# Kernel optimization log

Measured on AMD Instinct MI355X. Metric: run time of the kernel, lower is better.

The kernel has to match this reference:

```python
import jax, jax.numpy as jnp
import numpy as np

HEADS = 7
DIM_HEAD = 64
SCALE = DIM_HEAD ** -0.5


def setup_inputs() -> dict:
    key = jax.random.key(0)
    ks = jax.random.split(key, 6)
    b, n, dim = 8, 1024, 448
    inner = HEADS * DIM_HEAD  # 448
    x = jax.random.normal(ks[0], (b, n, dim), dtype=jnp.float32)
    w_qv = jax.random.normal(ks[1], (dim, 2 * inner), dtype=jnp.float32) * 0.02
    ext_k = jax.random.normal(ks[2], (HEADS, n, DIM_HEAD), dtype=jnp.float32)
    ext_bias = jax.random.normal(ks[3], (HEADS, n, n), dtype=jnp.float32)
    w_out = jax.random.normal(ks[4], (inner, dim), dtype=jnp.float32) * 0.02
    b_out = jnp.zeros((dim,), dtype=jnp.float32)
    return {"x": x, "w_qv": w_qv, "ext_k": ext_k, "ext_bias": ext_bias,
            "w_out": w_out, "b_out": b_out}


def reference(x, w_qv, ext_k, ext_bias, w_out, b_out):
    b, n, dim = x.shape
    qv = x @ w_qv                                   # [b, n, 2*inner]
    q, v = jnp.split(qv, 2, axis=-1)
    # b n (h d) -> b h n d
    q = q.reshape(b, n, HEADS, DIM_HEAD).transpose(0, 2, 1, 3)
    v = v.reshape(b, n, HEADS, DIM_HEAD).transpose(0, 2, 1, 3)
    # scores vs external learned key, additive bias applied BEFORE scale
    dots = (jnp.einsum('bhnd,hmd->bhnm', q, ext_k) + ext_bias[None]) * SCALE
    attn = jax.nn.softmax(dots, axis=-1)
    out = jnp.einsum('bhnm,bhmd->bhnd', attn, v)
    out = out.transpose(0, 2, 1, 3).reshape(b, n, HEADS * DIM_HEAD)
    return out @ w_out + b_out  # dropout is identity in eval mode
```

## Files before the change

kernel.cpp:

```cpp
#include <hip/hip_runtime.h>
#include <hip/hip_bf16.h>
#include <hip/hip_fp16.h>

#define BATCH 8
#define NSEQ 1024
#define DIMM 448
#define NHEAD 7
#define HDIM 64
#define MROWS (BATCH*NSEQ)
#define KDIM 448
#define SCALE_F 0.125f

typedef short short8 __attribute__((ext_vector_type(8)));
typedef float floatx16 __attribute__((ext_vector_type(16)));

#define MFMA32(a,b,c) __builtin_amdgcn_mfma_f32_32x32x16_bf16(a,b,c,0,0,0)

__device__ __forceinline__ unsigned short f2bf(float f){
    __hip_bfloat16 h = __float2bfloat16(f);
    return *reinterpret_cast<unsigned short*>(&h);
}
__device__ __forceinline__ float bf2f(unsigned short u){
    __hip_bfloat16 h; *reinterpret_cast<unsigned short*>(&h) = u;
    return __bfloat162float(h);
}
__device__ __forceinline__ float h2f(unsigned short u){
    __half h; *reinterpret_cast<unsigned short*>(&h) = u;
    return __half2float(h);
}
__device__ __forceinline__ unsigned short f2h(float f){
    __half h = __float2half(f);
    return *reinterpret_cast<unsigned short*>(&h);
}

__global__ __launch_bounds__(256)
void prep_all(const float* __restrict__ x, const float* __restrict__ ek,
              const float* __restrict__ wqv, const float* __restrict__ wout,
              const float* __restrict__ eb,
              unsigned short* __restrict__ xh, unsigned short* __restrict__ ekh,
              unsigned short* __restrict__ wqvTh, unsigned short* __restrict__ woTh,
              unsigned short* __restrict__ woTl, unsigned short* __restrict__ bp)
{
    __shared__ float T[2][64][33];
    const int bx = blockIdx.x, tid = threadIdx.x;

    if (bx < 3584) {
        int i = bx*256 + tid;
        float4 v = ((const float4*)x)[i];
        ((ushort4*)xh)[i] = make_ushort4(f2bf(v.x), f2bf(v.y), f2bf(v.z), f2bf(v.w));
    } else if (bx < 4032) {
        int i = (bx-3584)*256 + tid;
        float4 v = ((const float4*)ek)[i];
        ((ushort4*)ekh)[i] = make_ushort4(f2bf(v.x), f2bf(v.y), f2bf(v.z), f2bf(v.w));
    } else if (bx < 4228) {
        int lid = (bx-4032)*4 + (tid>>6);
        int kc = lid % 56, ng = lid / 56;
        int n = ng*64 + (tid&63);
        unsigned short h[8];
#pragma unroll
        for (int j = 0; j < 8; ++j) h[j] = f2bf(wqv[(size_t)(kc*8+j)*896 + n]);
        size_t o = (size_t)n*KDIM + kc*8;
        *(ushort4*)(wqvTh + o)     = make_ushort4(h[0],h[1],h[2],h[3]);
        *(ushort4*)(wqvTh + o + 4) = make_ushort4(h[4],h[5],h[6],h[7]);
    } else if (bx < 4340) {
        int lid = (bx-4228)*4 + (tid>>6);
        int kc = lid % 56, ng = lid / 56;
        int n = ng*64 + (tid&63);
        ushort4 h0={0,0,0,0}, h1={0,0,0,0}, l0={0,0,0,0}, l1={0,0,0,0};
        if (n < DIMM) {
            unsigned short h[8], l[8];
#pragma unroll
            for (int j = 0; j < 8; ++j) {
                float f = wout[(size_t)(kc*8+j)*DIMM + n];
                h[j] = f2bf(f); l[j] = f2bf(f - bf2f(h[j]));
            }
            h0 = make_ushort4(h[0],h[1],h[2],h[3]); h1 = make_ushort4(h[4],h[5],h[6],h[7]);
            l0 = make_ushort4(l[0],l[1],l[2],l[3]); l1 = make_ushort4(l[4],l[5],l[6],l[7]);
        }
        size_t o = (size_t)n*KDIM + kc*8;
        *(ushort4*)(woTh + o) = h0; *(ushort4*)(woTh + o + 4) = h1;
        *(ushort4*)(woTl + o) = l0; *(ushort4*)(woTl + o + 4) = l1;
    } else {
        const int sub = tid >> 7, st = tid & 127;
        const int lid = (bx-4340)*2 + sub;
        const int mt = lid & 31, qt = (lid>>5) & 15, h = lid >> 9;
#pragma unroll
        for (int it = 0; it < 4; ++it) {
            int idx = it*128 + st;
            int row = idx >> 3, c4 = (idx & 7)*4;
            float4 v = *(const float4*)(eb + ((size_t)(h*NSEQ + qt*64 + row))*NSEQ + mt*32 + c4);
            T[sub][row][c4+0]=v.x; T[sub][row][c4+1]=v.y;
            T[sub][row][c4+2]=v.z; T[sub][row][c4+3]=v.w;
        }
        __syncthreads();
        const int g2 = st >> 6, lane = st & 63;
        const int lq = lane & 31, quad = lane >> 5;
        const int q = g2*32 + lq;
        unsigned short* dst = bp + ((((size_t)h*16 + qt)*32 + mt)*4 + g2*2)*512 + lane*8;
#pragma unroll
        for (int jj = 0; jj < 2; ++jj) {
            unsigned short o[8];
#pragma unroll
            for (int t = 0; t < 8; ++t) {
                int m = (t&3) + 8*(t>>2) + 16*jj + 4*quad;
                o[t] = f2h(T[sub][q][m] * SCALE_F);
            }
            *(ushort4*)(dst + jj*512)     = make_ushort4(o[0],o[1],o[2],o[3]);
            *(ushort4*)(dst + jj*512 + 4) = make_ushort4(o[4],o[5],o[6],o[7]);
        }
    }
}

__global__ __launch_bounds__(64, 2)
void gemm1_reg(const unsigned short* __restrict__ Ah, const unsigned short* __restrict__ Bh,
               unsigned short* __restrict__ qd, unsigned short* __restrict__ vTd)
{
    const int lane = threadIdx.x;
    const int lq = lane & 31, lh = lane >> 5;
    const int m0 = blockIdx.x * 64;
    const int y  = blockIdx.y;
    const int n0 = y * 64;
    const unsigned short* aB = Ah + (size_t)(m0 + lq)*KDIM + lh*8;
    const unsigned short* bB = Bh + (size_t)(n0 + lq)*KDIM + lh*8;

    floatx16 acc[2][2] = {};
    short8 aR[2][2][2], bR[2][2][2];
#define LD1(kt, par) {                                                        \
    _Pragma("unroll") for (int fm = 0; fm < 2; ++fm)                          \
    _Pragma("unroll") for (int c = 0; c < 2; ++c) {                           \
        aR[par][fm][c] = *(const short8*)(aB + (size_t)fm*32*KDIM + (kt)*32 + c*16); \
        bR[par][fm][c] = *(const short8*)(bB + (size_t)fm*32*KDIM + (kt)*32 + c*16); } }

    LD1(0, 0)
#pragma unroll
    for (int kt = 0; kt < 14; ++kt) {
        const int par = kt & 1;
        if (kt < 13) LD1(kt+1, par^1)
#pragma unroll
        for (int c = 0; c < 2; ++c)
#pragma unroll
            for (int fm = 0; fm < 2; ++fm)
#pragma unroll
                for (int fn = 0; fn < 2; ++fn)
                    acc[fm][fn] = MFMA32(aR[par][fm][c], bR[par][fn][c], acc[fm][fn]);
    }
#undef LD1

    if (y < NHEAD) {
#pragma unroll
        for (int fm = 0; fm < 2; ++fm)
#pragma unroll
            for (int fn = 0; fn < 2; ++fn) {
                const int d = fn*32 + lq;
#pragma unroll
                for (int r = 0; r < 16; ++r) {
                    const int gm = m0 + fm*32 + (r&3) + 8*(r>>2) + 4*lh;
                    const int b = gm >> 10, ns = gm & 1023;
                    qd[((size_t)((b*NHEAD + y)*NSEQ + ns))*HDIM + d] = f2bf(acc[fm][fn][r]);
                }
            }
    } else {
        const int head = y - NHEAD;
#pragma unroll
        for (int fm = 0; fm < 2; ++fm)
#pragma unroll
            for (int fn = 0; fn < 2; ++fn) {
                const int d = fn*32 + lq;
#pragma unroll
                for (int r = 0; r < 16; ++r) {
                    const int gm = m0 + fm*32 + (r&3) + 8*(r>>2) + 4*lh;
                    const int b = gm >> 10, ns = gm & 1023;
                    vTd[((size_t)((b*NHEAD + head)*HDIM + d))*NSEQ + ns] = f2bf(acc[fm][fn][r]);
                }
            }
    }
}

__global__ __launch_bounds__(64, 2)
void attn4(const unsigned short* __restrict__ qh_g, const unsigned short* __restrict__ vTh,
           const unsigned short* __restrict__ ekh, const unsigned short* __restrict__ bp,
           unsigned short* __restrict__ aoh, unsigned short* __restrict__ aol)
{
    __shared__ unsigned short pS[1024];
    __shared__ float linv[2][32];

    const int lane = threadIdx.x;
    const int lq = lane & 31, lh = lane >> 5;
    const int qt = blockIdx.x, head = blockIdx.y, b = blockIdx.z;
    const int bh = b*NHEAD + head;

    short8 qf[2][4];
#pragma unroll
    for (int g2 = 0; g2 < 2; ++g2)
#pragma unroll
        for (int c = 0; c < 4; ++c)
            qf[g2][c] = *(const short8*)(qh_g +
                ((size_t)(bh*NSEQ) + qt*64 + g2*32 + lq)*HDIM + c*16 + lh*8);

    const unsigned short* kB = ekh + ((size_t)head*NSEQ + lq)*HDIM + lh*8;
    const unsigned short* vB = vTh + ((size_t)(bh*HDIM) + lq)*NSEQ;
    const unsigned short* bB = bp + ((size_t)(head*16 + qt))*65536 + lane*8;

    short8 kR[2][4], vR[2][4], bR[2][4];
#define PREF(J, par) { const int mm = ((J) < 32) ? (J) : 0;                    \
    _Pragma("unroll") for (int c = 0; c < 4; ++c)                              \
        kR[par][c] = *(const short8*)(kB + (size_t)mm*2048 + c*16);            \
    _Pragma("unroll") for (int c2 = 0; c2 < 2; ++c2)                           \
    _Pragma("unroll") for (int h2 = 0; h2 < 2; ++h2)                           \
        vR[par][c2*2+h2] = *(const short8*)(vB + (size_t)(h2*32)*NSEQ + mm*32 + (c2*2+lh)*8); \
    _Pragma("unroll") for (int u = 0; u < 4; ++u)                              \
        bR[par][u] = *(const short8*)(bB + ((size_t)mm*4 + u)*512); }

    floatx16 O[2][2] = {};
    float ls[2] = {0.f, 0.f};

#define SEC(J, par, nxt) {                                                     \
    PREF((J)+1, nxt)                                                           \
    _Pragma("unroll") for (int g2 = 0; g2 < 2; ++g2) {                         \
        floatx16 S = {};                                                       \
        _Pragma("unroll") for (int c = 0; c < 4; ++c)                          \
            S = MFMA32(kR[par][c], qf[g2][c], S);                              \
        _Pragma("unroll") for (int g = 0; g < 4; ++g) {                        \
            unsigned short hb[4];                                              \
            _Pragma("unroll") for (int j2 = 0; j2 < 4; ++j2) {                 \
                const int i = g*4 + j2;                                        \
                float bs = h2f((unsigned short)bR[par][g2*2 + (i>>3)][i&7]);   \
                float pv = __expf(fmaf(S[i], SCALE_F, bs));                    \
                ls[g2] += pv;  hb[j2] = f2bf(pv);                              \
            }                                                                  \
            *(ushort4*)(pS + g*256 + lq*8 + lh*4) = make_ushort4(hb[0],hb[1],hb[2],hb[3]); \
        }                                                                      \
        _Pragma("unroll") for (int c2 = 0; c2 < 2; ++c2) {                     \
            short8 pf = *(const short8*)(pS + ((c2*2+lh)*32 + lq)*8);          \
            O[g2][0] = MFMA32(pf, vR[par][c2*2+0], O[g2][0]);                  \
            O[g2][1] = MFMA32(pf, vR[par][c2*2+1], O[g2][1]);                  \
        } } }

    PREF(0, 0)
    for (int jj = 0; jj < 16; ++jj) {
        SEC(2*jj,   0, 1)
        SEC(2*jj+1, 1, 0)
    }
#undef SEC
#undef PREF

    float lt0 = ls[0] + __shfl_xor(ls[0], 32);
    float lt1 = ls[1] + __shfl_xor(ls[1], 32);
    if (lh == 0) { linv[0][lq] = 1.f/lt0; linv[1][lq] = 1.f/lt1; }

#pragma unroll
    for (int g2 = 0; g2 < 2; ++g2)
#pragma unroll
        for (int r = 0; r < 16; ++r) {
            const int qr = (r&3) + 8*(r>>2) + 4*lh;
            const float inv = linv[g2][qr];
            const size_t o = ((size_t)(b*NSEQ) + qt*64 + g2*32 + qr)*DIMM + head*HDIM + lq;
            float v0 = O[g2][0][r]*inv, v1 = O[g2][1][r]*inv;
            unsigned short h0 = f2bf(v0), h1 = f2bf(v1);
            aoh[o]      = h0;  aol[o]      = f2bf(v0 - bf2f(h0));
            aoh[o + 32] = h1;  aol[o + 32] = f2bf(v1 - bf2f(h1));
        }
}

__global__ __launch_bounds__(64, 2)
void gemm2_reg(const unsigned short* __restrict__ Ah, const unsigned short* __restrict__ Al,
               const unsigned short* __restrict__ Bh, const unsigned short* __restrict__ Bl,
               const float* __restrict__ bias, float* __restrict__ out)
{
    const int lane = threadIdx.x;
    const int lq = lane & 31, lh = lane >> 5;
    const int m0 = blockIdx.x * 64;
    const int n0 = blockIdx.y * 64;
    const unsigned short* aBh = Ah + (size_t)(m0 + lq)*KDIM + lh*8;
    const unsigned short* aBl = Al + (size_t)(m0 + lq)*KDIM + lh*8;
    const unsigned short* bBh = Bh + (size_t)(n0 + lq)*KDIM + lh*8;
    const unsigned short* bBl = Bl + (size_t)(n0 + lq)*KDIM + lh*8;

    floatx16 acc[2][2] = {};
    short8 aH[2][2][2], aL[2][2][2], bH[2][2][2], bL[2][2][2];
#define LD2(kt, par) {                                                        \
    _Pragma("unroll") for (int fm = 0; fm < 2; ++fm)                          \
    _Pragma("unroll") for (int c = 0; c < 2; ++c) {                           \
        const size_t off = (size_t)fm*32*KDIM + (kt)*32 + c*16;               \
        aH[par][fm][c] = *(const short8*)(aBh + off);                         \
        aL[par][fm][c] = *(const short8*)(aBl + off);                         \
        bH[par][fm][c] = *(const short8*)(bBh + off);                         \
        bL[par][fm][c] = *(const short8*)(bBl + off); } }

    LD2(0, 0)
#pragma unroll
    for (int kt = 0; kt < 14; ++kt) {
        const int par = kt & 1;
        if (kt < 13) LD2(kt+1, par^1)
#pragma unroll
        for (int c = 0; c < 2; ++c)
#pragma unroll
            for (int fm = 0; fm < 2; ++fm)
#pragma unroll
                for (int fn = 0; fn < 2; ++fn) {
                    acc[fm][fn] = MFMA32(aH[par][fm][c], bH[par][fn][c], acc[fm][fn]);
                    acc[fm][fn] = MFMA32(aL[par][fm][c], bH[par][fn][c], acc[fm][fn]);
                    acc[fm][fn] = MFMA32(aH[par][fm][c], bL[par][fn][c], acc[fm][fn]);
                }
    }
#undef LD2

#pragma unroll
    for (int fm = 0; fm < 2; ++fm)
#pragma unroll
        for (int fn = 0; fn < 2; ++fn) {
            const int gn = n0 + fn*32 + lq;
            const float bv = bias[gn];
#pragma unroll
            for (int r = 0; r < 16; ++r) {
                const int gm = m0 + fm*32 + (r&3) + 8*(r>>2) + 4*lh;
                out[(size_t)gm*DIMM + gn] = acc[fm][fn][r] + bv;
            }
        }
}

extern "C" void kernel_launch(void* const* d_in, const int* in_sizes, int n_in,
                              void* d_out, int out_size, void* d_ws, size_t ws_size,
                              hipStream_t stream)
{
    const float* x    = (const float*)d_in[0];
    const float* wqv  = (const float*)d_in[1];
    const float* ek   = (const float*)d_in[2];
    const float* eb   = (const float*)d_in[3];
    const float* wout = (const float*)d_in[4];
    const float* bout = (const float*)d_in[5];
    float* out = (float*)d_out;

    const size_t MK = (size_t)MROWS*KDIM;
    const size_t EK = (size_t)NHEAD*NSEQ*HDIM;
    unsigned short* p = (unsigned short*)d_ws;
    unsigned short* xh    = p;  p += MK;
    unsigned short* wqvTh = p;  p += (size_t)896*KDIM;
    unsigned short* woTh  = p;  p += (size_t)512*KDIM;
    unsigned short* woTl  = p;  p += (size_t)512*KDIM;
    unsigned short* ekh   = p;  p += EK;
    unsigned short* qh    = p;  p += MK;
    unsigned short* vTh   = p;  p += MK;
    unsigned short* bp    = p;  p += (size_t)NHEAD*NSEQ*NSEQ;
    unsigned short* aoh   = p;  p += MK;
    unsigned short* aol   = p;  p += MK;

    prep_all<<<6132, 256, 0, stream>>>(x, ek, wqv, wout, eb,
                                       xh, ekh, wqvTh, woTh, woTl, bp);
    gemm1_reg<<<dim3(128, 14), 64, 0, stream>>>(xh, wqvTh, qh, vTh);
    attn4<<<dim3(16, NHEAD, BATCH), 64, 0, stream>>>(qh, vTh, ekh, bp, aoh, aol);
    gemm2_reg<<<dim3(128, 7), 64, 0, stream>>>(aoh, aol, woTh, woTl, bout, out);
}
```

Measured before the change: 200.6 us.

## Split attention over key halves with combine pass, smaller GEMM tiles, shuffle-based P

Attention now splits the key dimension in two per 32-query tile. Each half writes unnormalized partial outputs and row sums, and a new combine kernel merges them and emits the hi/lo bf16 split. The P matrix is repacked through lane shuffles instead of shared memory, and prefetching is triple-buffered. Both GEMMs move to 32-row tiles, and gemm2 gains a two-wave split-K reduced through shared memory. The bias prepack layout and the w_out padding change to match. The goal is more parallel blocks and less LDS traffic, at the cost of an extra kernel launch and an fp32 partial-output round trip through memory.

Result: slower. 250.7 us (+24.9%).

```diff
diff --git a/kernel.cpp b/kernel.cpp
--- a/kernel.cpp
+++ b/kernel.cpp
@@ -10,9 +10,12 @@
 #define MROWS (BATCH*NSEQ)
 #define KDIM 448
 #define SCALE_F 0.125f
+#define NROW (56*NSEQ)
 
 typedef short short8 __attribute__((ext_vector_type(8)));
+typedef int   int4v  __attribute__((ext_vector_type(4)));
 typedef float floatx16 __attribute__((ext_vector_type(16)));
+typedef unsigned int u32;
 
 #define MFMA32(a,b,c) __builtin_amdgcn_mfma_f32_32x32x16_bf16(a,b,c,0,0,0)
 
@@ -31,6 +34,9 @@
 __device__ __forceinline__ unsigned short f2h(float f){
     __half h = __float2half(f);
     return *reinterpret_cast<unsigned short*>(&h);
+}
+__device__ __forceinline__ short8 i4_to_s8(int4v v){
+    union { int4v i; short8 s; } u; u.i = v; return u.s;
 }
 
 __global__ __launch_bounds__(256)
@@ -41,7 +47,7 @@
               unsigned short* __restrict__ wqvTh, unsigned short* __restrict__ woTh,
               unsigned short* __restrict__ woTl, unsigned short* __restrict__ bp)
 {
-    __shared__ float T[2][64][33];
+    __shared__ float T2[2][32][65];
     const int bx = blockIdx.x, tid = threadIdx.x;
 
     if (bx < 3584) {
@@ -62,261 +68,287 @@
         size_t o = (size_t)n*KDIM + kc*8;
         *(ushort4*)(wqvTh + o)     = make_ushort4(h[0],h[1],h[2],h[3]);
         *(ushort4*)(wqvTh + o + 4) = make_ushort4(h[4],h[5],h[6],h[7]);
-    } else if (bx < 4340) {
+    } else if (bx < 4326) {
         int lid = (bx-4228)*4 + (tid>>6);
         int kc = lid % 56, ng = lid / 56;
         int n = ng*64 + (tid&63);
-        ushort4 h0={0,0,0,0}, h1={0,0,0,0}, l0={0,0,0,0}, l1={0,0,0,0};
-        if (n < DIMM) {
-            unsigned short h[8], l[8];
-#pragma unroll
-            for (int j = 0; j < 8; ++j) {
-                float f = wout[(size_t)(kc*8+j)*DIMM + n];
-                h[j] = f2bf(f); l[j] = f2bf(f - bf2f(h[j]));
-            }
-            h0 = make_ushort4(h[0],h[1],h[2],h[3]); h1 = make_ushort4(h[4],h[5],h[6],h[7]);
-            l0 = make_ushort4(l[0],l[1],l[2],l[3]); l1 = make_ushort4(l[4],l[5],l[6],l[7]);
+        unsigned short h[8], l[8];
+#pragma unroll
+        for (int j = 0; j < 8; ++j) {
+            float f = wout[(size_t)(kc*8+j)*DIMM + n];
+            h[j] = f2bf(f); l[j] = f2bf(f - bf2f(h[j]));
         }
         size_t o = (size_t)n*KDIM + kc*8;
-        *(ushort4*)(woTh + o) = h0; *(ushort4*)(woTh + o + 4) = h1;
-        *(ushort4*)(woTl + o) = l0; *(ushort4*)(woTl + o + 4) = l1;
+        *(ushort4*)(woTh + o)     = make_ushort4(h[0],h[1],h[2],h[3]);
+        *(ushort4*)(woTh + o + 4) = make_ushort4(h[4],h[5],h[6],h[7]);
+        *(ushort4*)(woTl + o)     = make_ushort4(l[0],l[1],l[2],l[3]);
+        *(ushort4*)(woTl + o + 4) = make_ushort4(l[4],l[5],l[6],l[7]);
     } else {
         const int sub = tid >> 7, st = tid & 127;
-        const int lid = (bx-4340)*2 + sub;
-        const int mt = lid & 31, qt = (lid>>5) & 15, h = lid >> 9;
+        const int lid = (bx-4326)*2 + sub;
+        const int mtp = lid & 15, qt = (lid>>4) & 31, h = lid >> 9;
 #pragma unroll
         for (int it = 0; it < 4; ++it) {
             int idx = it*128 + st;
-            int row = idx >> 3, c4 = (idx & 7)*4;
-            float4 v = *(const float4*)(eb + ((size_t)(h*NSEQ + qt*64 + row))*NSEQ + mt*32 + c4);
-            T[sub][row][c4+0]=v.x; T[sub][row][c4+1]=v.y;
-            T[sub][row][c4+2]=v.z; T[sub][row][c4+3]=v.w;
+            int row = idx >> 4, c4 = (idx & 15)*4;
+            float4 v = *(const float4*)(eb + ((size_t)(h*NSEQ + qt*32 + row))*NSEQ
+                                           + mtp*64 + c4);
+            T2[sub][row][c4+0]=v.x; T2[sub][row][c4+1]=v.y;
+            T2[sub][row][c4+2]=v.z; T2[sub][row][c4+3]=v.w;
         }
         __syncthreads();
-        const int g2 = st >> 6, lane = st & 63;
-        const int lq = lane & 31, quad = lane >> 5;
-        const int q = g2*32 + lq;
-        unsigned short* dst = bp + ((((size_t)h*16 + qt)*32 + mt)*4 + g2*2)*512 + lane*8;
-#pragma unroll
-        for (int jj = 0; jj < 2; ++jj) {
-            unsigned short o[8];
-#pragma unroll
-            for (int t = 0; t < 8; ++t) {
-                int m = (t&3) + 8*(t>>2) + 16*jj + 4*quad;
-                o[t] = f2h(T[sub][q][m] * SCALE_F);
-            }
-            *(ushort4*)(dst + jj*512)     = make_ushort4(o[0],o[1],o[2],o[3]);
-            *(ushort4*)(dst + jj*512 + 4) = make_ushort4(o[4],o[5],o[6],o[7]);
-        }
-    }
-}
-
-__global__ __launch_bounds__(64, 2)
-void gemm1_reg(const unsigned short* __restrict__ Ah, const unsigned short* __restrict__ Bh,
-               unsigned short* __restrict__ qd, unsigned short* __restrict__ vTd)
+        const int half = st >> 6, slane = st & 63;
+        const int slq = slane & 31, slh = slane >> 5;
+        const int mt = mtp*2 + half;
+        unsigned short o[16];
+#pragma unroll
+        for (int g = 0; g < 4; ++g)
+#pragma unroll
+            for (int j = 0; j < 4; ++j)
+                o[g*4+j] = f2h(T2[sub][slq][half*32 + j + 8*g + 4*slh] * SCALE_F);
+        unsigned short* dst = bp + (((size_t)(h*32+qt))*32 + mt)*1024 + slane*16;
+        *(ushort4*)(dst+0)  = make_ushort4(o[0],o[1],o[2],o[3]);
+        *(ushort4*)(dst+4)  = make_ushort4(o[4],o[5],o[6],o[7]);
+        *(ushort4*)(dst+8)  = make_ushort4(o[8],o[9],o[10],o[11]);
+        *(ushort4*)(dst+12) = make_ushort4(o[12],o[13],o[14],o[15]);
+    }
+}
+
+__global__ __launch_bounds__(64, 4)
+void gemm1_r7(const unsigned short* __restrict__ Ah, const unsigned short* __restrict__ Bh,
+              unsigned short* __restrict__ qd, unsigned short* __restrict__ vTd)
 {
     const int lane = threadIdx.x;
     const int lq = lane & 31, lh = lane >> 5;
-    const int m0 = blockIdx.x * 64;
+    const int m0 = blockIdx.x * 32;
     const int y  = blockIdx.y;
     const int n0 = y * 64;
     const unsigned short* aB = Ah + (size_t)(m0 + lq)*KDIM + lh*8;
     const unsigned short* bB = Bh + (size_t)(n0 + lq)*KDIM + lh*8;
 
-    floatx16 acc[2][2] = {};
-    short8 aR[2][2][2], bR[2][2][2];
-#define LD1(kt, par) {                                                        \
-    _Pragma("unroll") for (int fm = 0; fm < 2; ++fm)                          \
-    _Pragma("unroll") for (int c = 0; c < 2; ++c) {                           \
-        aR[par][fm][c] = *(const short8*)(aB + (size_t)fm*32*KDIM + (kt)*32 + c*16); \
-        bR[par][fm][c] = *(const short8*)(bB + (size_t)fm*32*KDIM + (kt)*32 + c*16); } }
-
-    LD1(0, 0)
+    floatx16 acc[2] = {};
+    short8 aR[3][2], bR[3][4];
+#define LD1(kt, sl) {                                                          \
+    _Pragma("unroll") for (int c = 0; c < 2; ++c) {                            \
+        aR[sl][c] = *(const short8*)(aB + (kt)*32 + c*16);                     \
+        _Pragma("unroll") for (int fn = 0; fn < 2; ++fn)                       \
+            bR[sl][fn*2+c] = *(const short8*)(bB + (size_t)fn*32*KDIM + (kt)*32 + c*16); } }
+
+    LD1(0, 0) LD1(1, 1)
 #pragma unroll
     for (int kt = 0; kt < 14; ++kt) {
-        const int par = kt & 1;
-        if (kt < 13) LD1(kt+1, par^1)
+        if (kt < 12) LD1(kt+2, (kt+2)%3)
+        const int sl = kt % 3;
 #pragma unroll
         for (int c = 0; c < 2; ++c)
 #pragma unroll
-            for (int fm = 0; fm < 2; ++fm)
-#pragma unroll
-                for (int fn = 0; fn < 2; ++fn)
-                    acc[fm][fn] = MFMA32(aR[par][fm][c], bR[par][fn][c], acc[fm][fn]);
+            for (int fn = 0; fn < 2; ++fn)
+                acc[fn] = MFMA32(aR[sl][c], bR[sl][fn*2+c], acc[fn]);
     }
 #undef LD1
 
-    if (y < NHEAD) {
-#pragma unroll
-        for (int fm = 0; fm < 2; ++fm)
-#pragma unroll
-            for (int fn = 0; fn < 2; ++fn) {
-                const int d = fn*32 + lq;
-#pragma unroll
-                for (int r = 0; r < 16; ++r) {
-                    const int gm = m0 + fm*32 + (r&3) + 8*(r>>2) + 4*lh;
-                    const int b = gm >> 10, ns = gm & 1023;
-                    qd[((size_t)((b*NHEAD + y)*NSEQ + ns))*HDIM + d] = f2bf(acc[fm][fn][r]);
-                }
-            }
-    } else {
-        const int head = y - NHEAD;
-#pragma unroll
-        for (int fm = 0; fm < 2; ++fm)
-#pragma unroll
-            for (int fn = 0; fn < 2; ++fn) {
-                const int d = fn*32 + lq;
-#pragma unroll
-                for (int r = 0; r < 16; ++r) {
-                    const int gm = m0 + fm*32 + (r&3) + 8*(r>>2) + 4*lh;
-                    const int b = gm >> 10, ns = gm & 1023;
-                    vTd[((size_t)((b*NHEAD + head)*HDIM + d))*NSEQ + ns] = f2bf(acc[fm][fn][r]);
-                }
-            }
+#pragma unroll
+    for (int fn = 0; fn < 2; ++fn) {
+        const int gn = n0 + fn*32 + lq;
+        const int hcol = gn >> 6, d = gn & 63;
+#pragma unroll
+        for (int r = 0; r < 16; ++r) {
+            const int gm = m0 + (r&3) + 8*(r>>2) + 4*lh;
+            const int b = gm >> 10, ns = gm & 1023;
+            unsigned short h = f2bf(acc[fn][r]);
+            if (hcol < NHEAD)
+                qd[((size_t)((b*NHEAD + hcol)*NSEQ + ns))*HDIM + d] = h;
+            else
+                vTd[((size_t)((b*NHEAD + hcol - NHEAD)*HDIM + d))*NSEQ + ns] = h;
+        }
     }
 }
 
 __global__ __launch_bounds__(64, 2)
-void attn4(const unsigned short* __restrict__ qh_g, const unsigned short* __restrict__ vTh,
+void attn5(const unsigned short* __restrict__ qh_g, const unsigned short* __restrict__ vTh,
            const unsigned short* __restrict__ ekh, const unsigned short* __restrict__ bp,
-           unsigned short* __restrict__ aoh, unsigned short* __restrict__ aol)
-{
-    __shared__ unsigned short pS[1024];
-    __shared__ float linv[2][32];
-
+           float* __restrict__ pO, float* __restrict__ pl)
+{
     const int lane = threadIdx.x;
     const int lq = lane & 31, lh = lane >> 5;
-    const int qt = blockIdx.x, head = blockIdx.y, b = blockIdx.z;
+    const int qt = blockIdx.x & 31, ms = blockIdx.x >> 5;
+    const int head = blockIdx.y, b = blockIdx.z;
     const int bh = b*NHEAD + head;
-
-    short8 qf[2][4];
-#pragma unroll
-    for (int g2 = 0; g2 < 2; ++g2)
-#pragma unroll
-        for (int c = 0; c < 4; ++c)
-            qf[g2][c] = *(const short8*)(qh_g +
-                ((size_t)(bh*NSEQ) + qt*64 + g2*32 + lq)*HDIM + c*16 + lh*8);
+    const int ms16 = ms * 16;
+
+    short8 qf[4];
+#pragma unroll
+    for (int c = 0; c < 4; ++c)
+        qf[c] = *(const short8*)(qh_g +
+            ((size_t)(bh*NSEQ) + qt*32 + lq)*HDIM + c*16 + lh*8);
 
     const unsigned short* kB = ekh + ((size_t)head*NSEQ + lq)*HDIM + lh*8;
     const unsigned short* vB = vTh + ((size_t)(bh*HDIM) + lq)*NSEQ;
-    const unsigned short* bB = bp + ((size_t)(head*16 + qt))*65536 + lane*8;
-
-    short8 kR[2][4], vR[2][4], bR[2][4];
-#define PREF(J, par) { const int mm = ((J) < 32) ? (J) : 0;                    \
+    const unsigned short* bB = bp + ((size_t)(head*32 + qt))*32*1024 + lane*16;
+
+    short8 kR[3][4], vR[3][4], bR[3][2];
+#define PREF(J, sl) { const int mm = ms16 + (J);                               \
     _Pragma("unroll") for (int c = 0; c < 4; ++c)                              \
-        kR[par][c] = *(const short8*)(kB + (size_t)mm*2048 + c*16);            \
+        kR[sl][c] = *(const short8*)(kB + (size_t)mm*2048 + c*16);             \
+    _Pragma("unroll") for (int fn = 0; fn < 2; ++fn)                           \
     _Pragma("unroll") for (int c2 = 0; c2 < 2; ++c2)                           \
-    _Pragma("unroll") for (int h2 = 0; h2 < 2; ++h2)                           \
-        vR[par][c2*2+h2] = *(const short8*)(vB + (size_t)(h2*32)*NSEQ + mm*32 + (c2*2+lh)*8); \
-    _Pragma("unroll") for (int u = 0; u < 4; ++u)                              \
-        bR[par][u] = *(const short8*)(bB + ((size_t)mm*4 + u)*512); }
-
-    floatx16 O[2][2] = {};
-    float ls[2] = {0.f, 0.f};
-
-#define SEC(J, par, nxt) {                                                     \
-    PREF((J)+1, nxt)                                                           \
-    _Pragma("unroll") for (int g2 = 0; g2 < 2; ++g2) {                         \
-        floatx16 S = {};                                                       \
-        _Pragma("unroll") for (int c = 0; c < 4; ++c)                          \
-            S = MFMA32(kR[par][c], qf[g2][c], S);                              \
-        _Pragma("unroll") for (int g = 0; g < 4; ++g) {                        \
-            unsigned short hb[4];                                              \
-            _Pragma("unroll") for (int j2 = 0; j2 < 4; ++j2) {                 \
-                const int i = g*4 + j2;                                        \
-                float bs = h2f((unsigned short)bR[par][g2*2 + (i>>3)][i&7]);   \
-                float pv = __expf(fmaf(S[i], SCALE_F, bs));                    \
-                ls[g2] += pv;  hb[j2] = f2bf(pv);                              \
-            }                                                                  \
-            *(ushort4*)(pS + g*256 + lq*8 + lh*4) = make_ushort4(hb[0],hb[1],hb[2],hb[3]); \
-        }                                                                      \
-        _Pragma("unroll") for (int c2 = 0; c2 < 2; ++c2) {                     \
-            short8 pf = *(const short8*)(pS + ((c2*2+lh)*32 + lq)*8);          \
-            O[g2][0] = MFMA32(pf, vR[par][c2*2+0], O[g2][0]);                  \
-            O[g2][1] = MFMA32(pf, vR[par][c2*2+1], O[g2][1]);                  \
-        } } }
-
-    PREF(0, 0)
-    for (int jj = 0; jj < 16; ++jj) {
-        SEC(2*jj,   0, 1)
-        SEC(2*jj+1, 1, 0)
-    }
-#undef SEC
+        vR[sl][fn*2+c2] = *(const short8*)(vB + (size_t)(fn*32)*NSEQ + mm*32 + c2*16 + lh*8); \
+    bR[sl][0] = *(const short8*)(bB + (size_t)mm*1024);                        \
+    bR[sl][1] = *(const short8*)(bB + (size_t)mm*1024 + 8); }
+
+    floatx16 O[2] = {};
+    float ls = 0.f;
+
+    PREF(0, 0) PREF(1, 1)
+#pragma unroll
+    for (int sec = 0; sec < 16; ++sec) {
+        if (sec < 14) PREF(sec+2, (sec+2)%3)
+        const int sl = sec % 3;
+
+        floatx16 Sa = {}, Sb = {};
+        Sa = MFMA32(kR[sl][0], qf[0], Sa);
+        Sb = MFMA32(kR[sl][2], qf[2], Sb);
+        Sa = MFMA32(kR[sl][1], qf[1], Sa);
+        Sb = MFMA32(kR[sl][3], qf[3], Sb);
+
+        u32 Pq[4][2];
+#pragma unroll
+        for (int g = 0; g < 4; ++g) {
+            unsigned short hb[4];
+#pragma unroll
+            for (int j = 0; j < 4; ++j) {
+                const int r = g*4 + j;
+                float s = Sa[r] + Sb[r];
+                float bs = h2f((unsigned short)bR[sl][g>>1][(g&1)*4 + j]);
+                float pv = __expf(fmaf(s, SCALE_F, bs));
+                ls += pv;
+                hb[j] = f2bf(pv);
+            }
+            Pq[g][0] = (u32)hb[0] | ((u32)hb[1] << 16);
+            Pq[g][1] = (u32)hb[2] | ((u32)hb[3] << 16);
+        }
+        u32 pp[4][2];
+#pragma unroll
+        for (int g = 0; g < 4; ++g) {
+            pp[g][0] = (u32)__shfl_xor((int)Pq[g][0], 32);
+            pp[g][1] = (u32)__shfl_xor((int)Pq[g][1], 32);
+        }
+#pragma unroll
+        for (int c2 = 0; c2 < 2; ++c2) {
+            int4v iv;
+            iv.x = lh ? (int)pp[2*c2+1][0] : (int)Pq[2*c2][0];
+            iv.y = lh ? (int)pp[2*c2+1][1] : (int)Pq[2*c2][1];
+            iv.z = lh ? (int)Pq[2*c2+1][0] : (int)pp[2*c2][0];
+            iv.w = lh ? (int)Pq[2*c2+1][1] : (int)pp[2*c2][1];
+            short8 af = i4_to_s8(iv);
+            O[0] = MFMA32(af, vR[sl][0*2+c2], O[0]);
+            O[1] = MFMA32(af, vR[sl][1*2+c2], O[1]);
+        }
+    }
 #undef PREF
 
-    float lt0 = ls[0] + __shfl_xor(ls[0], 32);
-    float lt1 = ls[1] + __shfl_xor(ls[1], 32);
-    if (lh == 0) { linv[0][lq] = 1.f/lt0; linv[1][lq] = 1.f/lt1; }
-
-#pragma unroll
-    for (int g2 = 0; g2 < 2; ++g2)
+    float lt = ls + __shfl_xor(ls, 32);
+    if (lh == 0) pl[(size_t)(ms*56 + bh)*NSEQ + qt*32 + lq] = lt;
+
+    float* base = pO + ((size_t)(ms*56 + bh)*NSEQ + qt*32)*HDIM;
+#pragma unroll
+    for (int fn = 0; fn < 2; ++fn)
 #pragma unroll
         for (int r = 0; r < 16; ++r) {
             const int qr = (r&3) + 8*(r>>2) + 4*lh;
-            const float inv = linv[g2][qr];
-            const size_t o = ((size_t)(b*NSEQ) + qt*64 + g2*32 + qr)*DIMM + head*HDIM + lq;
-            float v0 = O[g2][0][r]*inv, v1 = O[g2][1][r]*inv;
-            unsigned short h0 = f2bf(v0), h1 = f2bf(v1);
-            aoh[o]      = h0;  aol[o]      = f2bf(v0 - bf2f(h0));
-            aoh[o + 32] = h1;  aol[o + 32] = f2bf(v1 - bf2f(h1));
-        }
-}
-
-__global__ __launch_bounds__(64, 2)
-void gemm2_reg(const unsigned short* __restrict__ Ah, const unsigned short* __restrict__ Al,
-               const unsigned short* __restrict__ Bh, const unsigned short* __restrict__ Bl,
-               const float* __restrict__ bias, float* __restrict__ out)
-{
-    const int lane = threadIdx.x;
+            base[(size_t)qr*HDIM + fn*32 + lq] = O[fn][r];
+        }
+}
+
+__global__ __launch_bounds__(256)
+void combine(const float* __restrict__ pO, const float* __restrict__ pl,
+             unsigned short* __restrict__ aoh, unsigned short* __restrict__ aol)
+{
+    const int idx = blockIdx.x*256 + threadIdx.x;
+    const int row = idx >> 4, d4 = (idx & 15) * 4;
+    const float inv = 1.0f / (pl[row] + pl[NROW + row]);
+    const float* p0 = pO + (size_t)row*HDIM + d4;
+    const float* p1 = p0 + (size_t)NROW*HDIM;
+    float4 a = *(const float4*)p0;
+    float4 c = *(const float4*)p1;
+    float v[4] = {(a.x+c.x)*inv, (a.y+c.y)*inv, (a.z+c.z)*inv, (a.w+c.w)*inv};
+    const int bh = row >> 10, q = row & 1023;
+    const int bi = bh / 7, head = bh - bi*7;
+    const size_t dst = ((size_t)(bi*NSEQ + q))*DIMM + head*HDIM + d4;
+    ushort4 h, l;
+    h.x = f2bf(v[0]); l.x = f2bf(v[0] - bf2f(h.x));
+    h.y = f2bf(v[1]); l.y = f2bf(v[1] - bf2f(h.y));
+    h.z = f2bf(v[2]); l.z = f2bf(v[2] - bf2f(h.z));
+    h.w = f2bf(v[3]); l.w = f2bf(v[3] - bf2f(h.w));
+    *(ushort4*)(aoh + dst) = h;
+    *(ushort4*)(aol + dst) = l;
+}
+
+__global__ __launch_bounds__(128, 3)
+void gemm2_r7(const unsigned short* __restrict__ Ah, const unsigned short* __restrict__ Al,
+              const unsigned short* __restrict__ Bh, const unsigned short* __restrict__ Bl,
+              const float* __restrict__ bias, float* __restrict__ out)
+{
+    __shared__ float sAcc[2048];
+    const int tid = threadIdx.x;
+    const int w = tid >> 6, lane = tid & 63;
     const int lq = lane & 31, lh = lane >> 5;
-    const int m0 = blockIdx.x * 64;
-    const int n0 = blockIdx.y * 64;
-    const unsigned short* aBh = Ah + (size_t)(m0 + lq)*KDIM + lh*8;
-    const unsigned short* aBl = Al + (size_t)(m0 + lq)*KDIM + lh*8;
-    const unsigned short* bBh = Bh + (size_t)(n0 + lq)*KDIM + lh*8;
-    const unsigned short* bBl = Bl + (size_t)(n0 + lq)*KDIM + lh*8;
-
-    floatx16 acc[2][2] = {};
-    short8 aH[2][2][2], aL[2][2][2], bH[2][2][2], bL[2][2][2];
-#define LD2(kt, par) {                                                        \
-    _Pragma("unroll") for (int fm = 0; fm < 2; ++fm)                          \
-    _Pragma("unroll") for (int c = 0; c < 2; ++c) {                           \
-        const size_t off = (size_t)fm*32*KDIM + (kt)*32 + c*16;               \
-        aH[par][fm][c] = *(const short8*)(aBh + off);                         \
-        aL[par][fm][c] = *(const short8*)(aBl + off);                         \
-        bH[par][fm][c] = *(const short8*)(bBh + off);                         \
-        bL[par][fm][c] = *(const short8*)(bBl + off); } }
+    const int m0 = blockIdx.x * 32, n0 = blockIdx.y * 64;
+    const int kb = w * 224;
+
+    const unsigned short* aBh = Ah + (size_t)(m0 + lq)*KDIM + kb + lh*8;
+    const unsigned short* aBl = Al + (size_t)(m0 + lq)*KDIM + kb + lh*8;
+    const unsigned short* bBh = Bh + (size_t)(n0 + lq)*KDIM + kb + lh*8;
+    const unsigned short* bBl = Bl + (size_t)(n0 + lq)*KDIM + kb + lh*8;
+
+    floatx16 acc[2] = {};
+    short8 aH[2][2], aL[2][2], bH[2][4], bL[2][4];
+#define LD2(kt, sl) {                                                          \
+    _Pragma("unroll") for (int c = 0; c < 2; ++c) {                            \
+        aH[sl][c] = *(const short8*)(aBh + (kt)*32 + c*16);                    \
+        aL[sl][c] = *(const short8*)(aBl + (kt)*32 + c*16);                    \
+        _Pragma("unroll") for (int fn = 0; fn < 2; ++fn) {                     \
+            bH[sl][fn*2+c] = *(const short8*)(bBh + (size_t)fn*32*KDIM + (kt)*32 + c*16); \
+            bL[sl][fn*2+c] = *(const short8*)(bBl + (size_t)fn*32*KDIM + (kt)*32 + c*16); } } }
 
     LD2(0, 0)
 #pragma unroll
-    for (int kt = 0; kt < 14; ++kt) {
-        const int par = kt & 1;
-        if (kt < 13) LD2(kt+1, par^1)
+    for (int kt = 0; kt < 7; ++kt) {
+        if (kt < 6) LD2(kt+1, (kt+1)&1)
+        const int sl = kt & 1;
 #pragma unroll
         for (int c = 0; c < 2; ++c)
 #pragma unroll
-            for (int fm = 0; fm < 2; ++fm)
-#pragma unroll
-                for (int fn = 0; fn < 2; ++fn) {
-                    acc[fm][fn] = MFMA32(aH[par][fm][c], bH[par][fn][c], acc[fm][fn]);
-                    acc[fm][fn] = MFMA32(aL[par][fm][c], bH[par][fn][c], acc[fm][fn]);
-                    acc[fm][fn] = MFMA32(aH[par][fm][c], bL[par][fn][c], acc[fm][fn]);
-                }
+            for (int fn = 0; fn < 2; ++fn) {
+                acc[fn] = MFMA32(aH[sl][c], bH[sl][fn*2+c], acc[fn]);
+                acc[fn] = MFMA32(aL[sl][c], bH[sl][fn*2+c], acc[fn]);
+                acc[fn] = MFMA32(aH[sl][c], bL[sl][fn*2+c], acc[fn]);
+            }
     }
 #undef LD2
 
-#pragma unroll
-    for (int fm = 0; fm < 2; ++fm)
+    if (w == 1) {
+#pragma unroll
+        for (int fn = 0; fn < 2; ++fn)
+#pragma unroll
+            for (int p4 = 0; p4 < 4; ++p4)
+                *(float4*)&sAcc[lane*32 + fn*16 + p4*4] =
+                    make_float4(acc[fn][p4*4], acc[fn][p4*4+1],
+                                acc[fn][p4*4+2], acc[fn][p4*4+3]);
+    }
+    __syncthreads();
+    if (w == 0) {
 #pragma unroll
         for (int fn = 0; fn < 2; ++fn) {
             const int gn = n0 + fn*32 + lq;
             const float bv = bias[gn];
 #pragma unroll
             for (int r = 0; r < 16; ++r) {
-                const int gm = m0 + fm*32 + (r&3) + 8*(r>>2) + 4*lh;
-                out[(size_t)gm*DIMM + gn] = acc[fm][fn][r] + bv;
+                const int gm = m0 + (r&3) + 8*(r>>2) + 4*lh;
+                out[(size_t)gm*DIMM + gn] = acc[fn][r] + sAcc[lane*32 + fn*16 + r] + bv;
             }
         }
+    }
 }
 
 extern "C" void kernel_launch(void* const* d_in, const int* in_sizes, int n_in,
@@ -336,18 +368,21 @@
     unsigned short* p = (unsigned short*)d_ws;
     unsigned short* xh    = p;  p += MK;
     unsigned short* wqvTh = p;  p += (size_t)896*KDIM;
-    unsigned short* woTh  = p;  p += (size_t)512*KDIM;
-    unsigned short* woTl  = p;  p += (size_t)512*KDIM;
+    unsigned short* woTh  = p;  p += (size_t)448*KDIM;
+    unsigned short* woTl  = p;  p += (size_t)448*KDIM;
     unsigned short* ekh   = p;  p += EK;
     unsigned short* qh    = p;  p += MK;
     unsigned short* vTh   = p;  p += MK;
     unsigned short* bp    = p;  p += (size_t)NHEAD*NSEQ*NSEQ;
-    unsigned short* aoh   = p;  p += MK;
     unsigned short* aol   = p;  p += MK;
-
-    prep_all<<<6132, 256, 0, stream>>>(x, ek, wqv, wout, eb,
+    float* pO = (float*)p;      p += 2*(size_t)NROW*HDIM*2;
+    float* pl = (float*)p;      p += 2*(size_t)NROW*2;
+    unsigned short* aoh = xh;
+
+    prep_all<<<6118, 256, 0, stream>>>(x, ek, wqv, wout, eb,
                                        xh, ekh, wqvTh, woTh, woTl, bp);
-    gemm1_reg<<<dim3(128, 14), 64, 0, stream>>>(xh, wqvTh, qh, vTh);
-    attn4<<<dim3(16, NHEAD, BATCH), 64, 0, stream>>>(qh, vTh, ekh, bp, aoh, aol);
-    gemm2_reg<<<dim3(128, 7), 64, 0, stream>>>(aoh, aol, woTh, woTl, bout, out);
-}
+    gemm1_r7<<<dim3(256, 14), 64, 0, stream>>>(xh, wqvTh, qh, vTh);
+    attn5<<<dim3(64, NHEAD, BATCH), 64, 0, stream>>>(qh, vTh, ekh, bp, pO, pl);
+    combine<<<3584, 256, 0, stream>>>(pO, pl, aoh, aol);
+    gemm2_r7<<<dim3(256, 7), 128, 0, stream>>>(aoh, aol, woTh, woTl, bout, out);
+}
```
